# Kernel optimization log

Hardware: AMD Instinct MI355X
Metric: run time of the kernel (lower is better)

The kernel has to match this reference:

```python
import jax, jax.numpy as jnp
import numpy as np
import math

B, N, M, D = 8, 2048, 2048, 512

def setup_inputs() -> dict:
    key = jax.random.key(0)
    ks = jax.random.split(key, 12)
    s = 1.0 / math.sqrt(D)
    return {
        "query_xyz": jax.random.normal(ks[0], (B, N, 3), jnp.float32),
        "query_feat": jax.random.normal(ks[1], (B, N, D), jnp.float32),
        "key_xyz": jax.random.normal(ks[2], (B, M, 3), jnp.float32),
        "key_feat": jax.random.normal(ks[3], (B, M, D), jnp.float32),
        "Wq": jax.random.normal(ks[4], (D, D), jnp.float32) * s,
        "bq": jnp.zeros((D,), jnp.float32),
        "Wk": jax.random.normal(ks[5], (D, D), jnp.float32) * s,
        "bk": jnp.zeros((D,), jnp.float32),
        "Wv": jax.random.normal(ks[6], (D, D), jnp.float32) * s,
        "bv": jnp.zeros((D,), jnp.float32),
        "Wo": jax.random.normal(ks[7], (D, D), jnp.float32) * s,
        "bo": jnp.zeros((D,), jnp.float32),
        "ln_g": jnp.ones((D,), jnp.float32),
        "ln_b": jnp.zeros((D,), jnp.float32),
    }

def reference(query_xyz, query_feat, key_xyz, key_feat,
              Wq, bq, Wk, bk, Wv, bv, Wo, bo, ln_g, ln_b):
    d = query_feat.shape[-1]
    # projections (torch Linear: x @ W.T + b)
    Q = jnp.einsum('bnd,ed->bne', query_feat, Wq) + bq
    K = jnp.einsum('bmd,ed->bme', key_feat, Wk) + bk
    V = jnp.einsum('bmd,ed->bme', key_feat, Wv) + bv
    scores = jnp.einsum('bnd,bmd->bnm', Q, K) / jnp.sqrt(jnp.float32(d))
    # pairwise euclidean distance via (||q||^2 + ||k||^2 - 2 q.k), avoids BxNxMx3
    qn = jnp.sum(query_xyz * query_xyz, axis=-1)  # [B,N]
    kn = jnp.sum(key_xyz * key_xyz, axis=-1)      # [B,M]
    d2 = qn[:, :, None] + kn[:, None, :] - 2.0 * jnp.einsum('bnc,bmc->bnm', query_xyz, key_xyz)
    dist = jnp.sqrt(jnp.maximum(d2, 1e-12))
    # distance bias: log(exp(-2*dist) + 1e-8)
    scores = scores + jnp.log(jnp.exp(-dist * 2.0) + 1e-8)
    attn = jax.nn.softmax(scores, axis=-1)
    # dropout is identity in eval mode
    attended = jnp.einsum('bnm,bme->bne', attn, V)
    out = jnp.einsum('bne,fe->bnf', attended, Wo) + bo
    x = query_feat + out
    # LayerNorm (eps=1e-5)
    mu = jnp.mean(x, axis=-1, keepdims=True)
    var = jnp.mean((x - mu) ** 2, axis=-1, keepdims=True)
    return (x - mu) * jax.lax.rsqrt(var + 1e-5) * ln_g + ln_b
```

## Files before the change

kernel.cpp:

```cpp
#include <hip/hip_runtime.h>

typedef __attribute__((ext_vector_type(8))) short short8;
typedef __attribute__((ext_vector_type(8))) unsigned short us8;
typedef __attribute__((ext_vector_type(4))) unsigned short us4;
typedef __attribute__((ext_vector_type(4))) float f32x4;

__device__ __forceinline__ float bf2f(unsigned short h) {
  return __uint_as_float(((unsigned int)h) << 16);
}
__device__ __forceinline__ unsigned short f2bf(float f) {
  unsigned int u = __float_as_uint(f);
  u += 0x7FFF + ((u >> 16) & 1);
  return (unsigned short)(u >> 16);
}

__device__ __forceinline__ void gload16(const void* g, void* l) {
  __builtin_amdgcn_global_load_lds(
      (const __attribute__((address_space(1))) unsigned int*)g,
      (__attribute__((address_space(3))) unsigned int*)l, 16, 0, 0);
}

#define BM 128
#define BN 128
#define BK 32

struct EpiParams {
  const float* bias;
  const float* aux0;
  const float* aux1;
  const void*  aux2;
  long  saux;
  float scale;
};

template<int EPI>
__global__ __launch_bounds__(256)
void gemm_bt(const unsigned short* __restrict__ A, const unsigned short* __restrict__ B,
             void* __restrict__ Cout, int Kd, int lda, int ldb, int ldc,
             long sA, long sB, long sC, EpiParams ep)
{
  __shared__ __attribute__((aligned(16))) char smem[16384];
  char* Al = smem;
  char* Bl = smem + 8192;

  const int t    = threadIdx.x;
  const int lane = t & 63;
  const int wid  = t >> 6;
  const int wr   = wid >> 1;
  const int wc   = wid & 1;
  const int tr   = lane & 15;
  const int tg   = lane >> 4;

  const int bz    = blockIdx.z;
  const int rbase = blockIdx.y * BM;
  const int cbase = blockIdx.x * BN;

  const unsigned short* Ab = A + (long)bz * sA;
  const unsigned short* Bb = B + (long)bz * sB;
  const char* Asrc = (const char*)(Ab + (long)rbase * lda);
  const char* Bsrc = (const char*)(Bb + (long)cbase * ldb);
  const long lda_b = (long)lda * 2;
  const long ldb_b = (long)ldb * 2;

  f32x4 acc[4][4] = {};

  for (int k0 = 0; k0 < Kd; k0 += BK) {
#pragma unroll
    for (int it = 0; it < 2; ++it) {
      const int boff = (it * 4 + wid) * 1024 + lane * 16;
      const int r  = boff >> 6;
      const int cb = boff & 63;
      gload16(Asrc + (long)r * lda_b + (k0 * 2 + cb), Al + (it * 4 + wid) * 1024);
      gload16(Bsrc + (long)r * ldb_b + (k0 * 2 + cb), Bl + (it * 4 + wid) * 1024);
    }
    __syncthreads();

    short8 af[4], bf[4];
#pragma unroll
    for (int m = 0; m < 4; ++m)
      af[m] = *(const short8*)(Al + ((wr * 64 + m * 16 + tr) * 32 + tg * 8) * 2);
#pragma unroll
    for (int n = 0; n < 4; ++n)
      bf[n] = *(const short8*)(Bl + ((wc * 64 + n * 16 + tr) * 32 + tg * 8) * 2);
#pragma unroll
    for (int m = 0; m < 4; ++m)
#pragma unroll
      for (int n = 0; n < 4; ++n)
        acc[m][n] = __builtin_amdgcn_mfma_f32_16x16x32_bf16(af[m], bf[n], acc[m][n], 0, 0, 0);
    __syncthreads();
  }

  if (EPI == 0) {
    unsigned short* C = (unsigned short*)Cout + (long)bz * sC;
#pragma unroll
    for (int n = 0; n < 4; ++n) {
      const int col = cbase + wc * 64 + n * 16 + tr;
      const float bv = ep.bias ? ep.bias[col] : 0.f;
#pragma unroll
      for (int m = 0; m < 4; ++m) {
#pragma unroll
        for (int i = 0; i < 4; ++i) {
          const int row = rbase + wr * 64 + m * 16 + tg * 4 + i;
          C[(long)row * ldc + col] = f2bf(acc[m][n][i] + bv);
        }
      }
    }
  } else if (EPI == 4) {
    if (cbase < 512) {
      unsigned short* C = (unsigned short*)Cout;
#pragma unroll
      for (int n = 0; n < 4; ++n) {
        const int col = cbase + wc * 64 + n * 16 + tr;
        const float bv = ep.bias[col];
#pragma unroll
        for (int m = 0; m < 4; ++m) {
#pragma unroll
          for (int i = 0; i < 4; ++i) {
            const int row = rbase + wr * 64 + m * 16 + tg * 4 + i;
            C[(long)row * 512 + col] = f2bf(acc[m][n][i] + bv);
          }
        }
      }
    } else {
      unsigned short* C = (unsigned short*)ep.aux2;
#pragma unroll
      for (int n = 0; n < 4; ++n) {
        const int e  = cbase - 512 + wc * 64 + n * 16 + tr;
        const float bv = ep.aux1[e];
#pragma unroll
        for (int m = 0; m < 4; ++m) {
          const int row0 = rbase + wr * 64 + m * 16 + tg * 4;
          const int b  = row0 >> 11;
          const int ml = row0 & 2047;
          us4 v;
#pragma unroll
          for (int i = 0; i < 4; ++i) v[i] = f2bf(acc[m][n][i] + bv);
          *(us4*)(C + ((long)b * 512 + e) * 2048 + ml) = v;
        }
      }
    }
  } else {
    float* C = (float*)Cout;
    const float* qf = ep.aux0;
#pragma unroll
    for (int n = 0; n < 4; ++n) {
      const int col = cbase + wc * 64 + n * 16 + tr;
      const float bv = ep.bias ? ep.bias[col] : 0.f;
#pragma unroll
      for (int m = 0; m < 4; ++m) {
#pragma unroll
        for (int i = 0; i < 4; ++i) {
          const int row = rbase + wr * 64 + m * 16 + tg * 4 + i;
          C[(long)row * 512 + col] = acc[m][n][i] + bv + qf[(long)row * 512 + col];
        }
      }
    }
  }
}

template<int EPI, int NWC>
__global__ __launch_bounds__(128 * NWC, 2)
void gemm_big(const unsigned short* __restrict__ A, const unsigned short* __restrict__ B,
              void* __restrict__ Cout, int Kd, int lda, int ldb, int ldc,
              long sA, long sB, long sC, int ntn, EpiParams ep)
{
  constexpr int T  = 128 * NWC;
  constexpr int NF = 128 / (NWC * 16);
  constexpr int RA = 16384 / (T * 16);
  constexpr int RB = 8192 / (T * 16);

  __shared__ __attribute__((aligned(16))) char smem[24576];
  char* Al = smem;
  char* Bl = smem + 16384;

  const int t    = threadIdx.x;
  const int lane = t & 63;
  const int wid  = t >> 6;
  const int wr   = wid / NWC;
  const int wc   = wid % NWC;
  const int tr   = lane & 15;
  const int tg   = lane >> 4;

  const int bz    = blockIdx.x;
  const int rbase = (blockIdx.y / ntn) * 256;
  const int cbase = (blockIdx.y % ntn) * 128;

  const unsigned short* Ab = A + (long)bz * sA;
  const unsigned short* Bb = B + (long)bz * sB;
  const char* Asrc = (const char*)(Ab + (long)rbase * lda);
  const char* Bsrc = (const char*)(Bb + (long)cbase * ldb);
  const long lda_b = (long)lda * 2;
  const long ldb_b = (long)ldb * 2;

  f32x4 acc[8][NF] = {};

  for (int k0 = 0; k0 < Kd; k0 += BK) {
#pragma unroll
    for (int r = 0; r < RA; ++r) {
      const int o = (r * T + t) * 16;
      gload16(Asrc + (long)(o >> 6) * lda_b + (k0 * 2 + (o & 63)),
              Al + (r * T + wid * 64) * 16);
    }
#pragma unroll
    for (int r = 0; r < RB; ++r) {
      const int o = (r * T + t) * 16;
      gload16(Bsrc + (long)(o >> 6) * ldb_b + (k0 * 2 + (o & 63)),
              Bl + (r * T + wid * 64) * 16);
    }
    __syncthreads();

    short8 af[8], bf[NF];
#pragma unroll
    for (int m = 0; m < 8; ++m)
      af[m] = *(const short8*)(Al + ((wr * 128 + m * 16 + tr) * 32 + tg * 8) * 2);
#pragma unroll
    for (int n = 0; n < NF; ++n)
      bf[n] = *(const short8*)(Bl + ((wc * (NF * 16) + n * 16 + tr) * 32 + tg * 8) * 2);
#pragma unroll
    for (int m = 0; m < 8; ++m)
#pragma unroll
      for (int n = 0; n < NF; ++n)
        acc[m][n] = __builtin_amdgcn_mfma_f32_16x16x32_bf16(af[m], bf[n], acc[m][n], 0, 0, 0);
    __syncthreads();
  }

  if (EPI == 0) {
    unsigned short* C = (unsigned short*)Cout + (long)bz * sC;
    const float* ls = (const float*)ep.aux2 + (long)bz * 2048 + rbase;
#pragma unroll
    for (int m = 0; m < 8; ++m) {
      const f32x4 lv = *(const f32x4*)(ls + wr * 128 + m * 16 + tg * 4);
      f32x4 inv;
#pragma unroll
      for (int i = 0; i < 4; ++i) inv[i] = 1.f / lv[i];
#pragma unroll
      for (int n = 0; n < NF; ++n) {
        const int col = cbase + wc * (NF * 16) + n * 16 + tr;
#pragma unroll
        for (int i = 0; i < 4; ++i) {
          const int row = rbase + wr * 128 + m * 16 + tg * 4 + i;
          C[(long)row * ldc + col] = f2bf(acc[m][n][i] * inv[i]);
        }
      }
    }
  } else {
    float* qs = (float*)smem;
    float* ks = (float*)smem + 768;
    {
      const float* q = ep.aux0 + (long)bz * ep.saux + (long)(rbase + t) * 3;
      qs[t * 3] = q[0]; qs[t * 3 + 1] = q[1]; qs[t * 3 + 2] = q[2];
      if (t < 128) {
        const float* k2 = ep.aux1 + (long)bz * ep.saux + (long)(cbase + t) * 3;
        ks[t * 3] = k2[0]; ks[t * 3 + 1] = k2[1]; ks[t * 3 + 2] = k2[2];
      }
    }
    __syncthreads();
    unsigned short* C = (unsigned short*)Cout + (long)bz * sC;
    float* lrow = (float*)ep.aux2 + (long)bz * 2048 + rbase;
    float ps[8][4];
#pragma unroll
    for (int m = 0; m < 8; ++m) {
#pragma unroll
      for (int i = 0; i < 4; ++i) {
        ps[m][i] = 0.f;
        const int rl = wr * 128 + m * 16 + tg * 4 + i;
        const float qx = qs[rl * 3], qy = qs[rl * 3 + 1], qz = qs[rl * 3 + 2];
#pragma unroll
        for (int n = 0; n < NF; ++n) {
          const int cl = wc * (NF * 16) + n * 16 + tr;
          const float dx = qx - ks[cl * 3];
          const float dy = qy - ks[cl * 3 + 1];
          const float dz = qz - ks[cl * 3 + 2];
          const float d2 = dx * dx + dy * dy + dz * dz;
          const float d  = sqrtf(fmaxf(d2, 1e-12f));
          const float bias = fmaxf(-2.f * d, -18.420680743952367f);
          const float p = __expf(acc[m][n][i] * ep.scale + bias - 5.f);
          ps[m][i] += p;
          C[(long)(rbase + rl) * ldc + (cbase + cl)] = f2bf(p);
        }
      }
    }
#pragma unroll
    for (int off = 1; off <= 8; off <<= 1)
#pragma unroll
      for (int m = 0; m < 8; ++m)
#pragma unroll
        for (int i = 0; i < 4; ++i)
          ps[m][i] += __shfl_xor(ps[m][i], off, 64);
    if (tr == 0) {
#pragma unroll
      for (int m = 0; m < 8; ++m)
#pragma unroll
        for (int i = 0; i < 4; ++i)
          atomicAdd(&lrow[wr * 128 + m * 16 + tg * 4 + i], ps[m][i]);
    }
  }
}

__global__ __launch_bounds__(256)
void ln_rows(const float* __restrict__ X, const float* __restrict__ g,
             const float* __restrict__ b, float* __restrict__ O)
{
  const int row  = blockIdx.x * 4 + (threadIdx.x >> 6);
  const int lane = threadIdx.x & 63;
  const float* xp = X + (long)row * 512;

  f32x4 v0 = *(const f32x4*)(xp + lane * 4);
  f32x4 v1 = *(const f32x4*)(xp + 256 + lane * 4);

  float s = 0.f;
#pragma unroll
  for (int j = 0; j < 4; ++j) s += v0[j] + v1[j];
#pragma unroll
  for (int off = 32; off; off >>= 1) s += __shfl_xor(s, off, 64);
  const float mu = s * (1.f / 512.f);

  float vs = 0.f;
#pragma unroll
  for (int j = 0; j < 4; ++j) {
    float d0 = v0[j] - mu, d1 = v1[j] - mu;
    vs += d0 * d0 + d1 * d1;
  }
#pragma unroll
  for (int off = 32; off; off >>= 1) vs += __shfl_xor(vs, off, 64);
  const float r = rsqrtf(vs * (1.f / 512.f) + 1e-5f);

  f32x4 g0 = *(const f32x4*)(g + lane * 4);
  f32x4 g1 = *(const f32x4*)(g + 256 + lane * 4);
  f32x4 b0 = *(const f32x4*)(b + lane * 4);
  f32x4 b1 = *(const f32x4*)(b + 256 + lane * 4);

  f32x4 o0, o1;
#pragma unroll
  for (int j = 0; j < 4; ++j) {
    o0[j] = (v0[j] - mu) * r * g0[j] + b0[j];
    o1[j] = (v1[j] - mu) * r * g1[j] + b1[j];
  }
  float* op = O + (long)row * 512;
  *(f32x4*)(op + lane * 4) = o0;
  *(f32x4*)(op + 256 + lane * 4) = o1;
}

__global__ __launch_bounds__(256)
void cvt_feat(const float* __restrict__ a, const float* __restrict__ b,
              unsigned short* __restrict__ oa, unsigned short* __restrict__ ob)
{
  const float* src = blockIdx.y ? b : a;
  unsigned short* dst = blockIdx.y ? ob : oa;
  const long i = blockIdx.x * 256 + threadIdx.x;
  const f32x4* s = (const f32x4*)src;
  f32x4 x = s[i * 2];
  f32x4 y = s[i * 2 + 1];
  us8 o;
#pragma unroll
  for (int j = 0; j < 4; ++j) { o[j] = f2bf(x[j]); o[4 + j] = f2bf(y[j]); }
  *(us8*)(dst + i * 8) = o;
}

__global__ __launch_bounds__(256)
void cvt_w(const float* __restrict__ w0, const float* __restrict__ w1,
           const float* __restrict__ w2, const float* __restrict__ w3,
           unsigned short* __restrict__ dst)
{
  const float* src = blockIdx.y == 0 ? w0 : blockIdx.y == 1 ? w1 : blockIdx.y == 2 ? w2 : w3;
  unsigned short* d = dst + (long)blockIdx.y * 262144;
  const long i = blockIdx.x * 256 + threadIdx.x;
  const f32x4* s = (const f32x4*)src;
  f32x4 x = s[i * 2];
  f32x4 y = s[i * 2 + 1];
  us8 o;
#pragma unroll
  for (int j = 0; j < 4; ++j) { o[j] = f2bf(x[j]); o[4 + j] = f2bf(y[j]); }
  *(us8*)(d + i * 8) = o;
}

extern "C" void kernel_launch(void* const* d_in, const int* in_sizes, int n_in,
                              void* d_out, int out_size, void* d_ws, size_t ws_size,
                              hipStream_t stream)
{
  const float* qxyz  = (const float*)d_in[0];
  const float* qfeat = (const float*)d_in[1];
  const float* kxyz  = (const float*)d_in[2];
  const float* kfeat = (const float*)d_in[3];
  const float* Wq = (const float*)d_in[4];
  const float* bq = (const float*)d_in[5];
  const float* Wk = (const float*)d_in[6];
  const float* bk = (const float*)d_in[7];
  const float* Wv = (const float*)d_in[8];
  const float* bv = (const float*)d_in[9];
  const float* Wo = (const float*)d_in[10];
  const float* bo = (const float*)d_in[11];
  const float* lng = (const float*)d_in[12];
  const float* lnb = (const float*)d_in[13];

  const long SZ_FEAT = 16777216;
  char* ws = (char*)d_ws;
  if (ws_size < (size_t)153092096) return;

  unsigned short* XQ  = (unsigned short*)(ws);
  unsigned short* XK  = (unsigned short*)(ws + SZ_FEAT);
  unsigned short* QB  = (unsigned short*)(ws + 2 * SZ_FEAT);
  unsigned short* KB  = (unsigned short*)(ws + 3 * SZ_FEAT);
  unsigned short* VT  = (unsigned short*)(ws + 4 * SZ_FEAT);
  unsigned short* WQB = (unsigned short*)(ws + 5 * SZ_FEAT);
  unsigned short* WKB = WQB + 262144;
  unsigned short* WOB = WQB + 786432;
  unsigned short* SB  = (unsigned short*)(ws + 5 * SZ_FEAT + 2097152);
  unsigned short* ATT = QB;
  float* XRES = (float*)ws;
  float* LSUM = (float*)(ws + SZ_FEAT);

  cvt_feat<<<dim3(4096, 2), 256, 0, stream>>>(qfeat, kfeat, XQ, XK);
  cvt_w<<<dim3(128, 4), 256, 0, stream>>>(Wq, Wk, Wv, Wo, WQB);

  EpiParams e0{}; e0.bias = bq;
  gemm_bt<0><<<dim3(4, 128, 1), 256, 0, stream>>>(XQ, WQB, QB, 512, 512, 512, 512, 0, 0, 0, e0);
  EpiParams e1{}; e1.bias = bk; e1.aux1 = bv; e1.aux2 = VT;
  gemm_bt<4><<<dim3(8, 128, 1), 256, 0, stream>>>(XK, WKB, KB, 512, 512, 512, 512, 0, 0, 0, e1);

  hipMemsetAsync(LSUM, 0, 8 * 2048 * sizeof(float), stream);

  EpiParams es{}; es.aux0 = qxyz; es.aux1 = kxyz; es.aux2 = LSUM; es.saux = 2048 * 3;
  es.scale = 0.044194173824159216f;
  gemm_big<2, 2><<<dim3(8, 128), 256, 0, stream>>>(QB, KB, SB, 512, 512, 512, 2048,
                                                   (long)2048 * 512, (long)2048 * 512,
                                                   (long)2048 * 2048, 16, es);

  EpiParams ep{}; ep.aux2 = LSUM;
  gemm_big<0, 4><<<dim3(8, 32), 512, 0, stream>>>(SB, VT, ATT, 2048, 2048, 2048, 512,
                                                  (long)2048 * 2048, (long)512 * 2048,
                                                  (long)2048 * 512, 4, ep);

  EpiParams eo{}; eo.bias = bo; eo.aux0 = qfeat;
  gemm_bt<3><<<dim3(4, 128, 1), 256, 0, stream>>>(ATT, WOB, XRES, 512, 512, 512, 512, 0, 0, 0, eo);

  ln_rows<<<4096, 256, 0, stream>>>(XRES, lng, lnb, (float*)d_out);
}
```

Baseline: 277.2 us.

## Replace big GEMM with double-buffered, XOR-swizzled 128x256 tile kernel

```diff
diff --git a/kernel.cpp b/kernel.cpp
--- a/kernel.cpp
+++ b/kernel.cpp
@@ -158,119 +158,131 @@
   }
 }
 
-template<int EPI, int NWC>
-__global__ __launch_bounds__(128 * NWC, 2)
-void gemm_big(const unsigned short* __restrict__ A, const unsigned short* __restrict__ B,
-              void* __restrict__ Cout, int Kd, int lda, int ldb, int ldc,
-              long sA, long sB, long sC, int ntn, EpiParams ep)
-{
-  constexpr int T  = 128 * NWC;
-  constexpr int NF = 128 / (NWC * 16);
-  constexpr int RA = 16384 / (T * 16);
-  constexpr int RB = 8192 / (T * 16);
-
-  __shared__ __attribute__((aligned(16))) char smem[24576];
-  char* Al = smem;
-  char* Bl = smem + 16384;
+template<int EPI>
+__global__ __launch_bounds__(512, 2)
+void gemm2(const unsigned short* __restrict__ A, const unsigned short* __restrict__ B,
+           void* __restrict__ Cout, int Kd, int lda, int ldb, int ldc,
+           long sA, long sB, long sC, int ntn, EpiParams ep)
+{
+  __shared__ __attribute__((aligned(16))) char smem[98304];
 
   const int t    = threadIdx.x;
   const int lane = t & 63;
   const int wid  = t >> 6;
-  const int wr   = wid / NWC;
-  const int wc   = wid % NWC;
+  const int wr   = wid >> 2;
+  const int wc   = wid & 3;
   const int tr   = lane & 15;
   const int tg   = lane >> 4;
 
   const int bz    = blockIdx.x;
-  const int rbase = (blockIdx.y / ntn) * 256;
-  const int cbase = (blockIdx.y % ntn) * 128;
-
-  const unsigned short* Ab = A + (long)bz * sA;
-  const unsigned short* Bb = B + (long)bz * sB;
-  const char* Asrc = (const char*)(Ab + (long)rbase * lda);
-  const char* Bsrc = (const char*)(Bb + (long)cbase * ldb);
+  const int rbase = (blockIdx.y / ntn) * 128;
+  const int cbase = (blockIdx.y % ntn) * 256;
+
   const long lda_b = (long)lda * 2;
   const long ldb_b = (long)ldb * 2;
-
-  f32x4 acc[8][NF] = {};
-
-  for (int k0 = 0; k0 < Kd; k0 += BK) {
-#pragma unroll
-    for (int r = 0; r < RA; ++r) {
-      const int o = (r * T + t) * 16;
-      gload16(Asrc + (long)(o >> 6) * lda_b + (k0 * 2 + (o & 63)),
-              Al + (r * T + wid * 64) * 16);
-    }
-#pragma unroll
-    for (int r = 0; r < RB; ++r) {
-      const int o = (r * T + t) * 16;
-      gload16(Bsrc + (long)(o >> 6) * ldb_b + (k0 * 2 + (o & 63)),
-              Bl + (r * T + wid * 64) * 16);
+  const char* Asrc = (const char*)(A + (long)bz * sA + (long)rbase * lda);
+  const char* Bsrc = (const char*)(B + (long)bz * sB + (long)cbase * ldb);
+
+  const int srow   = t >> 3;
+  const int scol16 = (t & 7) ^ ((t >> 3) & 7);
+  const char* gA[2];
+  const char* gB[4];
+#pragma unroll
+  for (int c = 0; c < 2; ++c)
+    gA[c] = Asrc + (long)(c * 64 + srow) * lda_b + scol16 * 16;
+#pragma unroll
+  for (int c = 0; c < 4; ++c)
+    gB[c] = Bsrc + (long)(c * 64 + srow) * ldb_b + scol16 * 16;
+
+  f32x4 acc[4][4] = {};
+  const int NT = Kd >> 6;
+  int slot = 0;
+
+#pragma unroll
+  for (int c = 0; c < 2; ++c) gload16(gA[c], smem + c * 8192 + wid * 1024);
+#pragma unroll
+  for (int c = 0; c < 4; ++c) gload16(gB[c], smem + 16384 + c * 8192 + wid * 1024);
+  __syncthreads();
+
+  for (int tk = 0; tk < NT; ++tk) {
+    if (tk + 1 < NT) {
+      const int so = (slot ^ 1) * 49152;
+      const long adv = (long)(tk + 1) * 128;
+#pragma unroll
+      for (int c = 0; c < 2; ++c) gload16(gA[c] + adv, smem + so + c * 8192 + wid * 1024);
+#pragma unroll
+      for (int c = 0; c < 4; ++c) gload16(gB[c] + adv, smem + so + 16384 + c * 8192 + wid * 1024);
+    }
+    const char* As = smem + slot * 49152;
+    const char* Bs = As + 16384;
+    const int x7 = tr & 7;
+#pragma unroll
+    for (int ks = 0; ks < 2; ++ks) {
+      const int coff = ((ks * 4 + tg) ^ x7) * 16;
+      short8 af[4], bf[4];
+#pragma unroll
+      for (int m = 0; m < 4; ++m)
+        af[m] = *(const short8*)(As + (wr * 64 + m * 16 + tr) * 128 + coff);
+#pragma unroll
+      for (int n = 0; n < 4; ++n)
+        bf[n] = *(const short8*)(Bs + (wc * 64 + n * 16 + tr) * 128 + coff);
+#pragma unroll
+      for (int m = 0; m < 4; ++m)
+#pragma unroll
+        for (int n = 0; n < 4; ++n)
+          acc[m][n] = __builtin_amdgcn_mfma_f32_16x16x32_bf16(af[m], bf[n], acc[m][n], 0, 0, 0);
     }
     __syncthreads();
-
-    short8 af[8], bf[NF];
-#pragma unroll
-    for (int m = 0; m < 8; ++m)
-      af[m] = *(const short8*)(Al + ((wr * 128 + m * 16 + tr) * 32 + tg * 8) * 2);
-#pragma unroll
-    for (int n = 0; n < NF; ++n)
-      bf[n] = *(const short8*)(Bl + ((wc * (NF * 16) + n * 16 + tr) * 32 + tg * 8) * 2);
-#pragma unroll
-    for (int m = 0; m < 8; ++m)
-#pragma unroll
-      for (int n = 0; n < NF; ++n)
-        acc[m][n] = __builtin_amdgcn_mfma_f32_16x16x32_bf16(af[m], bf[n], acc[m][n], 0, 0, 0);
-    __syncthreads();
+    slot ^= 1;
   }
 
   if (EPI == 0) {
     unsigned short* C = (unsigned short*)Cout + (long)bz * sC;
-    const float* ls = (const float*)ep.aux2 + (long)bz * 2048 + rbase;
-#pragma unroll
-    for (int m = 0; m < 8; ++m) {
-      const f32x4 lv = *(const f32x4*)(ls + wr * 128 + m * 16 + tg * 4);
+    const float* ls = (const float*)ep.aux2 + (long)bz * 2048 + rbase + wr * 64;
+#pragma unroll
+    for (int m = 0; m < 4; ++m) {
+      const f32x4 lv = *(const f32x4*)(ls + m * 16 + tg * 4);
       f32x4 inv;
 #pragma unroll
       for (int i = 0; i < 4; ++i) inv[i] = 1.f / lv[i];
 #pragma unroll
-      for (int n = 0; n < NF; ++n) {
-        const int col = cbase + wc * (NF * 16) + n * 16 + tr;
+      for (int n = 0; n < 4; ++n) {
+        const int col = cbase + wc * 64 + n * 16 + tr;
 #pragma unroll
         for (int i = 0; i < 4; ++i) {
-          const int row = rbase + wr * 128 + m * 16 + tg * 4 + i;
+          const int row = rbase + wr * 64 + m * 16 + tg * 4 + i;
           C[(long)row * ldc + col] = f2bf(acc[m][n][i] * inv[i]);
         }
       }
     }
   } else {
-    float* qs = (float*)smem;
-    float* ks = (float*)smem + 768;
-    {
+    float* qs  = (float*)smem;
+    float* ks2 = (float*)smem + 384;
+    if (t < 128) {
       const float* q = ep.aux0 + (long)bz * ep.saux + (long)(rbase + t) * 3;
       qs[t * 3] = q[0]; qs[t * 3 + 1] = q[1]; qs[t * 3 + 2] = q[2];
-      if (t < 128) {
-        const float* k2 = ep.aux1 + (long)bz * ep.saux + (long)(cbase + t) * 3;
-        ks[t * 3] = k2[0]; ks[t * 3 + 1] = k2[1]; ks[t * 3 + 2] = k2[2];
-      }
+    } else if (t < 384) {
+      const int tt = t - 128;
+      const float* k2 = ep.aux1 + (long)bz * ep.saux + (long)(cbase + tt) * 3;
+      ks2[tt * 3] = k2[0]; ks2[tt * 3 + 1] = k2[1]; ks2[tt * 3 + 2] = k2[2];
     }
     __syncthreads();
     unsigned short* C = (unsigned short*)Cout + (long)bz * sC;
     float* lrow = (float*)ep.aux2 + (long)bz * 2048 + rbase;
-    float ps[8][4];
-#pragma unroll
-    for (int m = 0; m < 8; ++m) {
+    float ps[4][4];
+#pragma unroll
+    for (int m = 0; m < 4; ++m) {
 #pragma unroll
       for (int i = 0; i < 4; ++i) {
         ps[m][i] = 0.f;
-        const int rl = wr * 128 + m * 16 + tg * 4 + i;
+        const int rl = wr * 64 + m * 16 + tg * 4 + i;
         const float qx = qs[rl * 3], qy = qs[rl * 3 + 1], qz = qs[rl * 3 + 2];
 #pragma unroll
-        for (int n = 0; n < NF; ++n) {
-          const int cl = wc * (NF * 16) + n * 16 + tr;
-          const float dx = qx - ks[cl * 3];
-          const float dy = qy - ks[cl * 3 + 1];
-          const float dz = qz - ks[cl * 3 + 2];
+        for (int n = 0; n < 4; ++n) {
+          const int cl = wc * 64 + n * 16 + tr;
+          const float dx = qx - ks2[cl * 3];
+          const float dy = qy - ks2[cl * 3 + 1];
+          const float dz = qz - ks2[cl * 3 + 2];
           const float d2 = dx * dx + dy * dy + dz * dz;
           const float d  = sqrtf(fmaxf(d2, 1e-12f));
           const float bias = fmaxf(-2.f * d, -18.420680743952367f);
@@ -283,16 +295,16 @@
 #pragma unroll
     for (int off = 1; off <= 8; off <<= 1)
 #pragma unroll
-      for (int m = 0; m < 8; ++m)
+      for (int m = 0; m < 4; ++m)
 #pragma unroll
         for (int i = 0; i < 4; ++i)
           ps[m][i] += __shfl_xor(ps[m][i], off, 64);
     if (tr == 0) {
 #pragma unroll
-      for (int m = 0; m < 8; ++m)
+      for (int m = 0; m < 4; ++m)
 #pragma unroll
         for (int i = 0; i < 4; ++i)
-          atomicAdd(&lrow[wr * 128 + m * 16 + tg * 4 + i], ps[m][i]);
+          atomicAdd(&lrow[wr * 64 + m * 16 + tg * 4 + i], ps[m][i]);
     }
   }
 }
@@ -422,14 +434,14 @@
 
   EpiParams es{}; es.aux0 = qxyz; es.aux1 = kxyz; es.aux2 = LSUM; es.saux = 2048 * 3;
   es.scale = 0.044194173824159216f;
-  gemm_big<2, 2><<<dim3(8, 128), 256, 0, stream>>>(QB, KB, SB, 512, 512, 512, 2048,
-                                                   (long)2048 * 512, (long)2048 * 512,
-                                                   (long)2048 * 2048, 16, es);
+  gemm2<2><<<dim3(8, 128), 512, 0, stream>>>(QB, KB, SB, 512, 512, 512, 2048,
+                                             (long)2048 * 512, (long)2048 * 512,
+                                             (long)2048 * 2048, 8, es);
 
   EpiParams ep{}; ep.aux2 = LSUM;
-  gemm_big<0, 4><<<dim3(8, 32), 512, 0, stream>>>(SB, VT, ATT, 2048, 2048, 2048, 512,
-                                                  (long)2048 * 2048, (long)512 * 2048,
-                                                  (long)2048 * 512, 4, ep);
+  gemm2<0><<<dim3(8, 32), 512, 0, stream>>>(SB, VT, ATT, 2048, 2048, 2048, 512,
+                                            (long)2048 * 2048, (long)512 * 2048,
+                                            (long)2048 * 512, 2, ep);
 
   EpiParams eo{}; eo.bias = bo; eo.aux0 = qfeat;
   gemm_bt<3><<<dim3(4, 128, 1), 256, 0, stream>>>(ATT, WOB, XRES, 512, 512, 512, 512, 0, 0, 0, eo);
```

Measured after the change: 261.5 us. 1.06x faster.

## Fold output projection into value projection by precomputing Wo·Wv

Applied to the files above, without the earlier changes.

```diff
diff --git a/kernel.cpp b/kernel.cpp
--- a/kernel.cpp
+++ b/kernel.cpp
@@ -105,7 +105,7 @@
         }
       }
     }
-  } else if (EPI == 4) {
+  } else {
     if (cbase < 512) {
       unsigned short* C = (unsigned short*)Cout;
 #pragma unroll
@@ -136,22 +136,6 @@
 #pragma unroll
           for (int i = 0; i < 4; ++i) v[i] = f2bf(acc[m][n][i] + bv);
           *(us4*)(C + ((long)b * 512 + e) * 2048 + ml) = v;
-        }
-      }
-    }
-  } else {
-    float* C = (float*)Cout;
-    const float* qf = ep.aux0;
-#pragma unroll
-    for (int n = 0; n < 4; ++n) {
-      const int col = cbase + wc * 64 + n * 16 + tr;
-      const float bv = ep.bias ? ep.bias[col] : 0.f;
-#pragma unroll
-      for (int m = 0; m < 4; ++m) {
-#pragma unroll
-        for (int i = 0; i < 4; ++i) {
-          const int row = rbase + wr * 64 + m * 16 + tg * 4 + i;
-          C[(long)row * 512 + col] = acc[m][n][i] + bv + qf[(long)row * 512 + col];
         }
       }
     }
@@ -225,8 +209,9 @@
   }
 
   if (EPI == 0) {
-    unsigned short* C = (unsigned short*)Cout + (long)bz * sC;
+    float* C = (float*)Cout + (long)bz * sC;
     const float* ls = (const float*)ep.aux2 + (long)bz * 2048 + rbase;
+    const float* qf = ep.aux0;
 #pragma unroll
     for (int m = 0; m < 8; ++m) {
       const f32x4 lv = *(const f32x4*)(ls + wr * 128 + m * 16 + tg * 4);
@@ -236,10 +221,12 @@
 #pragma unroll
       for (int n = 0; n < NF; ++n) {
         const int col = cbase + wc * (NF * 16) + n * 16 + tr;
+        const float bb = ep.bias[col];
 #pragma unroll
         for (int i = 0; i < 4; ++i) {
           const int row = rbase + wr * 128 + m * 16 + tg * 4 + i;
-          C[(long)row * ldc + col] = f2bf(acc[m][n][i] * inv[i]);
+          C[(long)row * ldc + col] =
+              acc[m][n][i] * inv[i] + bb + qf[((long)bz * 2048 + row) * 512 + col];
         }
       }
     }
@@ -372,6 +359,45 @@
 #pragma unroll
   for (int j = 0; j < 4; ++j) { o[j] = f2bf(x[j]); o[4 + j] = f2bf(y[j]); }
   *(us8*)(d + i * 8) = o;
+}
+
+__global__ __launch_bounds__(256)
+void cvt_wT(const float* __restrict__ Wv, unsigned short* __restrict__ WvT)
+{
+  __shared__ float tile[64 * 68];
+  const int t = threadIdx.x;
+  const int e0 = blockIdx.y * 64, d0 = blockIdx.x * 64;
+#pragma unroll
+  for (int c = 0; c < 4; ++c) {
+    const int L = c * 256 + t;
+    const int r = L >> 4, g = L & 15;
+    const f32x4 v = *(const f32x4*)(Wv + (long)(e0 + r) * 512 + d0 + g * 4);
+    *(f32x4*)(tile + r * 68 + g * 4) = v;
+  }
+  __syncthreads();
+#pragma unroll
+  for (int c = 0; c < 2; ++c) {
+    const int L = c * 256 + t;
+    const int d = L >> 3, ge = L & 7;
+    us8 o;
+#pragma unroll
+    for (int j = 0; j < 8; ++j) o[j] = f2bf(tile[(ge * 8 + j) * 68 + d]);
+    *(us8*)(WvT + (long)(d0 + d) * 512 + e0 + ge * 8) = o;
+  }
+}
+
+__global__ __launch_bounds__(256)
+void bvo_k(const float* __restrict__ Wo, const float* __restrict__ bv,
+           float* __restrict__ out)
+{
+  const int f = blockIdx.x * 256 + threadIdx.x;
+  float s = 0.f;
+  for (int e = 0; e < 512; e += 4) {
+    const f32x4 w = *(const f32x4*)(Wo + (long)f * 512 + e);
+    const f32x4 b = *(const f32x4*)(bv + e);
+    s += w[0] * b[0] + w[1] * b[1] + w[2] * b[2] + w[3] * b[3];
+  }
+  out[f] = s;
 }
 
 extern "C" void kernel_launch(void* const* d_in, const int* in_sizes, int n_in,
@@ -404,18 +430,25 @@
   unsigned short* VT  = (unsigned short*)(ws + 4 * SZ_FEAT);
   unsigned short* WQB = (unsigned short*)(ws + 5 * SZ_FEAT);
   unsigned short* WKB = WQB + 262144;
+  unsigned short* WVO = WQB + 524288;
   unsigned short* WOB = WQB + 786432;
   unsigned short* SB  = (unsigned short*)(ws + 5 * SZ_FEAT + 2097152);
-  unsigned short* ATT = QB;
+  unsigned short* WVT = SB;
+  float* BVO  = (float*)((char*)SB + 524288);
   float* XRES = (float*)ws;
-  float* LSUM = (float*)(ws + SZ_FEAT);
+  float* LSUM = (float*)(WOB);
 
   cvt_feat<<<dim3(4096, 2), 256, 0, stream>>>(qfeat, kfeat, XQ, XK);
   cvt_w<<<dim3(128, 4), 256, 0, stream>>>(Wq, Wk, Wv, Wo, WQB);
+  cvt_wT<<<dim3(8, 8), 256, 0, stream>>>(Wv, WVT);
+  bvo_k<<<dim3(2), 256, 0, stream>>>(Wo, bv, BVO);
+
+  EpiParams ew{};
+  gemm_bt<0><<<dim3(4, 4, 1), 256, 0, stream>>>(WOB, WVT, WVO, 512, 512, 512, 512, 0, 0, 0, ew);
 
   EpiParams e0{}; e0.bias = bq;
   gemm_bt<0><<<dim3(4, 128, 1), 256, 0, stream>>>(XQ, WQB, QB, 512, 512, 512, 512, 0, 0, 0, e0);
-  EpiParams e1{}; e1.bias = bk; e1.aux1 = bv; e1.aux2 = VT;
+  EpiParams e1{}; e1.bias = bk; e1.aux1 = BVO; e1.aux2 = VT;
   gemm_bt<4><<<dim3(8, 128, 1), 256, 0, stream>>>(XK, WKB, KB, 512, 512, 512, 512, 0, 0, 0, e1);
 
   hipMemsetAsync(LSUM, 0, 8 * 2048 * sizeof(float), stream);
@@ -426,13 +459,10 @@
                                                    (long)2048 * 512, (long)2048 * 512,
                                                    (long)2048 * 2048, 16, es);
 
-  EpiParams ep{}; ep.aux2 = LSUM;
-  gemm_big<0, 4><<<dim3(8, 32), 512, 0, stream>>>(SB, VT, ATT, 2048, 2048, 2048, 512,
+  EpiParams ep{}; ep.aux2 = LSUM; ep.bias = bo; ep.aux0 = qfeat;
+  gemm_big<0, 4><<<dim3(8, 32), 512, 0, stream>>>(SB, VT, XRES, 2048, 2048, 2048, 512,
                                                   (long)2048 * 2048, (long)512 * 2048,
                                                   (long)2048 * 512, 4, ep);
 
-  EpiParams eo{}; eo.bias = bo; eo.aux0 = qfeat;
-  gemm_bt<3><<<dim3(4, 128, 1), 256, 0, stream>>>(ATT, WOB, XRES, 512, 512, 512, 512, 0, 0, 0, eo);
-
   ln_rows<<<4096, 256, 0, stream>>>(XRES, lng, lnb, (float*)d_out);
 }
```

Result: slower. 287.6 us (+3.7%).
